# Optimization experiments

Hardware: AMD Instinct MI355X
Metric: run time of the kernel (lower is better)

## Reference

```python
import jax, jax.numpy as jnp
import numpy as np

BN_EPS = 1e-3
BN_SCALE = 1.0 / np.sqrt(1.0 + BN_EPS)  # inference BN with default moving stats (mean=0, var=1)


def _gru(x_seq, h0, Wx, Wh, b):
    """Keras GRU (reset_after=True). x_seq: [B,T,in], h0: [B,u].
    Wx: [in,3u], Wh: [u,3u], b: [2,3u] (input bias, recurrent bias).
    Returns (outputs [B,T,u], h_T [B,u])."""
    # precompute input contributions for all timesteps in one big matmul
    xg = jnp.einsum('bti,ig->btg', x_seq, Wx) + b[0]  # [B,T,3u]
    xg = jnp.moveaxis(xg, 1, 0)  # [T,B,3u] for scan

    def step(h, xt):
        rg = h @ Wh + b[1]  # [B,3u]
        xz, xr, xh = jnp.split(xt, 3, axis=-1)
        rz, rr, rh = jnp.split(rg, 3, axis=-1)
        z = jax.nn.sigmoid(xz + rz)
        r = jax.nn.sigmoid(xr + rr)
        hh = jnp.tanh(xh + r * rh)
        hn = z * h + (1.0 - z) * hh
        return hn, hn

    hT, ys = jax.lax.scan(step, h0, xg)
    return jnp.moveaxis(ys, 0, 1), hT  # [B,T,u], [B,u]


def _encoder(x_ids, h0, E, params):
    xcur = E[x_ids]  # [B,T,d]
    new_hidden = []
    out = xcur
    for i, (Wxf, Whf, bf, Wxb, Whb, bb) in enumerate(params):
        fw_out, fw_h = _gru(xcur, h0[i, 0], Wxf, Whf, bf)
        bw_out, bw_h = _gru(xcur[:, ::-1, :], h0[i, 1], Wxb, Whb, bb)
        # BN(training=False) with fresh layers == scale by 1/sqrt(1+eps)
        out = jnp.concatenate([fw_out * BN_SCALE, bw_out * BN_SCALE], axis=2)
        new_hidden.append(jnp.stack([fw_h, bw_h], axis=0))
        xcur = out
    # final BN on each direction hidden state
    new_hidden = jnp.stack(new_hidden, axis=0) * BN_SCALE  # [L,2,B,u]
    return out, new_hidden


def setup_inputs() -> dict:
    key = jax.random.key(0)
    ks = jax.random.split(key, 16)
    B, T, V, D, U = 32, 256, 32000, 512, 512
    s = 0.1
    inp = {
        'x': jax.random.randint(ks[0], (B, T), 0, V, dtype=jnp.int64)
             if jax.config.jax_enable_x64 else jax.random.randint(ks[0], (B, T), 0, V, dtype=jnp.int32),
        'h0': jnp.zeros((2, 2, B, U), jnp.float32),
        'E': jax.random.normal(ks[1], (V, D), jnp.float32) * s,
        'Wx0f': jax.random.normal(ks[2], (D, 3 * U), jnp.float32) * s,
        'Wh0f': jax.random.normal(ks[3], (U, 3 * U), jnp.float32) * s,
        'b0f': jax.random.normal(ks[4], (2, 3 * U), jnp.float32) * s,
        'Wx0b': jax.random.normal(ks[5], (D, 3 * U), jnp.float32) * s,
        'Wh0b': jax.random.normal(ks[6], (U, 3 * U), jnp.float32) * s,
        'b0b': jax.random.normal(ks[7], (2, 3 * U), jnp.float32) * s,
        'Wx1f': jax.random.normal(ks[8], (2 * U, 3 * U), jnp.float32) * s,
        'Wh1f': jax.random.normal(ks[9], (U, 3 * U), jnp.float32) * s,
        'b1f': jax.random.normal(ks[10], (2, 3 * U), jnp.float32) * s,
        'Wx1b': jax.random.normal(ks[11], (2 * U, 3 * U), jnp.float32) * s,
        'Wh1b': jax.random.normal(ks[12], (U, 3 * U), jnp.float32) * s,
        'b1b': jax.random.normal(ks[13], (2, 3 * U), jnp.float32) * s,
    }
    return inp


def reference(x, h0, E, Wx0f, Wh0f, b0f, Wx0b, Wh0b, b0b,
              Wx1f, Wh1f, b1f, Wx1b, Wh1b, b1b):
    params = [(Wx0f, Wh0f, b0f, Wx0b, Wh0b, b0b),
              (Wx1f, Wh1f, b1f, Wx1b, Wh1b, b1b)]
    return _encoder(x, h0, E, params)
```

## Files before the change

kernel.cpp:

```cpp
#include <hip/hip_runtime.h>
#include <hip/hip_bf16.h>


typedef __attribute__((ext_vector_type(8))) short short8;
typedef __attribute__((ext_vector_type(8))) __bf16 bf16x8;
typedef __attribute__((ext_vector_type(4))) float f32x4;
typedef __attribute__((ext_vector_type(4))) int i32x4;
typedef __attribute__((ext_vector_type(2))) float f32x2;

#define DEVINLINE __device__ __forceinline__

static constexpr int B = 32, T = 256, U = 512, NG = 1536;
static constexpr int BU = B * U;
static constexpr long OUT_ELEMS = 8388608;
static constexpr float SCALE_BN = 0.9995003746879552f;

DEVINLINE unsigned bfbits(float f) {
  unsigned u = __float_as_uint(f);
  return (u + 0x7fffu + ((u >> 16) & 1u)) >> 16;
}
DEVINLINE float bf2f(unsigned bits) { return __uint_as_float(bits << 16); }
DEVINLINE void split2(float v, unsigned& hi, unsigned& lo) {
  hi = bfbits(v);
  lo = bfbits(v - bf2f(hi));
}
DEVINLINE float sigmoidf_(float x) { return 1.f / (1.f + __expf(-x)); }
DEVINLINE float tanhf_(float x) {
  x = fminf(15.f, fmaxf(-15.f, x));
  float e = __expf(2.f * x);
  return (e - 1.f) / (e + 1.f);
}
DEVINLINE f32x4 mfma16(short8 a, short8 b, f32x4 c) {
  return __builtin_amdgcn_mfma_f32_16x16x32_bf16(
      __builtin_bit_cast(bf16x8, a), __builtin_bit_cast(bf16x8, b), c, 0, 0, 0);
}

__global__ __launch_bounds__(256)
void transpose_w(const float* __restrict__ in, unsigned short* __restrict__ oh,
                 unsigned short* __restrict__ ol, int K, int N) {
  __shared__ float tile[32][33];
  const int n0 = blockIdx.x * 32, k0 = blockIdx.y * 32;
  const int tx = threadIdx.x & 31, ty = threadIdx.x >> 5;
  for (int i = ty; i < 32; i += 8)
    tile[i][tx] = in[(long)(k0 + i) * N + n0 + tx];
  __syncthreads();
  for (int i = ty; i < 32; i += 8) {
    const float v = tile[tx][i];
    unsigned hi, lo;
    split2(v, hi, lo);
    oh[(long)(n0 + i) * K + k0 + tx] = (unsigned short)hi;
    ol[(long)(n0 + i) * K + k0 + tx] = (unsigned short)lo;
  }
}

__global__ __launch_bounds__(256)
void embed_kernel(const int* __restrict__ x, const float* __restrict__ E,
                  unsigned short* __restrict__ xh, unsigned short* __restrict__ xl) {
  const int r = blockIdx.x;
  const int t = r >> 5, b = r & 31;
  const int id = x[b * T + t];
  const float* src = E + (long)id * 512;
  f32x2 v = *reinterpret_cast<const f32x2*>(src + threadIdx.x * 2);
  unsigned h0, l0, h1, l1;
  split2(v.x, h0, l0);
  split2(v.y, h1, l1);
  ((unsigned*)xh)[(long)r * 256 + threadIdx.x] = h0 | (h1 << 16);
  ((unsigned*)xl)[(long)r * 256 + threadIdx.x] = l0 | (l1 << 16);
}

template <int K>
__global__ __launch_bounds__(256)
void gemm_bias(const unsigned short* __restrict__ Ah,
               const unsigned short* __restrict__ Al,
               const unsigned short* __restrict__ Bh,
               const unsigned short* __restrict__ Bl,
               const float* __restrict__ bias, float* __restrict__ C) {
  __shared__ __align__(16) unsigned short AsH[128 * 32];
  __shared__ __align__(16) unsigned short BsH[128 * 32];
  __shared__ __align__(16) unsigned short AsL[128 * 32];
  __shared__ __align__(16) unsigned short BsL[128 * 32];
  const int m0 = blockIdx.x * 128, n0 = blockIdx.y * 128;
  const int tid = threadIdx.x, lane = tid & 63, wave = tid >> 6;
  const int wr = wave >> 1, wc = wave & 1, lr = lane & 15, kq = lane >> 4;
  f32x4 acc[4][4] = {};
  for (int kt = 0; kt < K / 32; ++kt) {
    const int k0 = kt * 32;
    i32x4 vah[2], vbh[2], val[2], vbl[2];
#pragma unroll
    for (int u = 0; u < 2; ++u) {
      const int idx = tid + u * 256, row = idx >> 2, sub = idx & 3;
      vah[u] = *reinterpret_cast<const i32x4*>(Ah + (long)(m0 + row) * K + k0 + sub * 8);
      vbh[u] = *reinterpret_cast<const i32x4*>(Bh + (long)(n0 + row) * K + k0 + sub * 8);
      val[u] = *reinterpret_cast<const i32x4*>(Al + (long)(m0 + row) * K + k0 + sub * 8);
      vbl[u] = *reinterpret_cast<const i32x4*>(Bl + (long)(n0 + row) * K + k0 + sub * 8);
    }
    __syncthreads();
#pragma unroll
    for (int u = 0; u < 2; ++u) {
      const int idx = tid + u * 256;
      *reinterpret_cast<i32x4*>(AsH + idx * 8) = vah[u];
      *reinterpret_cast<i32x4*>(BsH + idx * 8) = vbh[u];
      *reinterpret_cast<i32x4*>(AsL + idx * 8) = val[u];
      *reinterpret_cast<i32x4*>(BsL + idx * 8) = vbl[u];
    }
    __syncthreads();
    short8 afh[4], bfh[4], afl[4], bfl[4];
#pragma unroll
    for (int i = 0; i < 4; ++i) {
      afh[i] = *reinterpret_cast<const short8*>(AsH + (wr * 64 + i * 16 + lr) * 32 + kq * 8);
      bfh[i] = *reinterpret_cast<const short8*>(BsH + (wc * 64 + i * 16 + lr) * 32 + kq * 8);
      afl[i] = *reinterpret_cast<const short8*>(AsL + (wr * 64 + i * 16 + lr) * 32 + kq * 8);
      bfl[i] = *reinterpret_cast<const short8*>(BsL + (wc * 64 + i * 16 + lr) * 32 + kq * 8);
    }
#pragma unroll
    for (int i = 0; i < 4; ++i)
#pragma unroll
      for (int j = 0; j < 4; ++j) {
        acc[i][j] = mfma16(afh[i], bfh[j], acc[i][j]);
        acc[i][j] = mfma16(afh[i], bfl[j], acc[i][j]);
        acc[i][j] = mfma16(afl[i], bfh[j], acc[i][j]);
      }
  }
#pragma unroll
  for (int j = 0; j < 4; ++j) {
    const int col = n0 + wc * 64 + j * 16 + lr;
    const float bv = bias[col];
#pragma unroll
    for (int i = 0; i < 4; ++i) {
      const int row0 = m0 + wr * 64 + i * 16 + kq * 4;
#pragma unroll
      for (int r = 0; r < 4; ++r)
        C[(long)(row0 + r) * NG + col] = acc[i][j][r] + bv;
    }
  }
}

__global__ __launch_bounds__(384, 1)
void gru_scan(const float* __restrict__ xgf, const float* __restrict__ xgb,
              const unsigned short* __restrict__ whtfh,
              const unsigned short* __restrict__ whtfl,
              const unsigned short* __restrict__ whtbh,
              const unsigned short* __restrict__ whtbl,
              const float* __restrict__ rbf, const float* __restrict__ rbb,
              const float* __restrict__ h0L,
              unsigned short* __restrict__ hbh,
              unsigned short* __restrict__ hbl,
              int* __restrict__ flags,
              unsigned short* __restrict__ out0h,
              unsigned short* __restrict__ out0l,
              float* __restrict__ outF,
              float* __restrict__ hT,
              const int layer) {
  const int dir = blockIdx.x >> 4, wg = blockIdx.x & 15;
  const int j0 = wg * 32;
  const int tid = threadIdx.x, wave = tid >> 6, lane = tid & 63;
  const int lr = lane & 15, kq = lane >> 4;
  const float* xg = dir ? xgb : xgf;
  const unsigned short* wth = dir ? whtbh : whtfh;
  const unsigned short* wtl = dir ? whtbl : whtfl;
  const float* rb = dir ? rbb : rbf;
  const float* h0d = h0L + dir * BU;
  unsigned short* hbhd = hbh + dir * 2 * BU;
  unsigned short* hbld = hbl + dir * 2 * BU;
  int* flg = flags + dir * 16;

  __shared__ __align__(16) unsigned short h_hi[32][520];
  __shared__ __align__(16) unsigned short h_lo[32][520];
  __shared__ float rg_lds[32][97];

  const int g = wave >> 1, half = wave & 1;
  const int c0 = g * 512 + j0 + half * 16;
  short8 wfh[16], wfl[16];
#pragma unroll
  for (int kk = 0; kk < 16; ++kk) {
    wfh[kk] = *reinterpret_cast<const short8*>(wth + (long)(c0 + lr) * 512 + kk * 32 + kq * 8);
    wfl[kk] = *reinterpret_cast<const short8*>(wtl + (long)(c0 + lr) * 512 + kk * 32 + kq * 8);
  }
  const float bv = rb[c0 + lr];

  float hpr[2][2];
#pragma unroll
  for (int q = 0; q < 2; ++q) {
    const int p = tid + q * 384;
    if (p < 512) {
      const int b = p >> 4, jr = (p & 15) * 2;
      hpr[q][0] = h0d[b * U + j0 + jr];
      hpr[q][1] = h0d[b * U + j0 + jr + 1];
    }
  }

  for (int s = 0; s < T; ++s) {
    const int t_in = dir ? (T - 1 - s) : s;
    const int par = s & 1;

    f32x2 xv[2][3];
    {
      const long xbase = (long)t_in * 32 * NG;
#pragma unroll
      for (int q = 0; q < 2; ++q) {
        const int p = tid + q * 384;
        if (p < 512) {
          const int b = p >> 4, jr = (p & 15) * 2;
#pragma unroll
          for (int gg = 0; gg < 3; ++gg)
            xv[q][gg] = *reinterpret_cast<const f32x2*>(
                xg + xbase + (long)b * NG + gg * 512 + j0 + jr);
        }
      }
    }

    if (s == 0) {
      for (int p = tid; p < BU / 4; p += 384) {
        const int b = p >> 7, u = (p & 127) * 4;
        f32x4 v = *reinterpret_cast<const f32x4*>(h0d + b * U + u);
        unsigned hi0, lo0, hi1, lo1, hi2, lo2, hi3, lo3;
        split2(v.x, hi0, lo0); split2(v.y, hi1, lo1);
        split2(v.z, hi2, lo2); split2(v.w, hi3, lo3);
        unsigned* dh = reinterpret_cast<unsigned*>(&h_hi[b][u]);
        unsigned* dl = reinterpret_cast<unsigned*>(&h_lo[b][u]);
        dh[0] = hi0 | (hi1 << 16); dh[1] = hi2 | (hi3 << 16);
        dl[0] = lo0 | (lo1 << 16); dl[1] = lo2 | (lo3 << 16);
      }
    } else {
      const unsigned short* hsh = hbhd + par * BU;
      const unsigned short* hsl = hbld + par * BU;
      for (int p = tid; p < BU / 8; p += 384) {
        const int b = p >> 6, u = (p & 63) * 8;
        *reinterpret_cast<i32x4*>(&h_hi[b][u]) =
            *reinterpret_cast<const i32x4*>(hsh + b * U + u);
        *reinterpret_cast<i32x4*>(&h_lo[b][u]) =
            *reinterpret_cast<const i32x4*>(hsl + b * U + u);
      }
    }
    __syncthreads();

    f32x4 aHH0 = {}, aHL0 = {}, aLH0 = {}, aHH1 = {}, aHL1 = {}, aLH1 = {};
#pragma unroll
    for (int kk = 0; kk < 16; ++kk) {
      const short8 a0h = *reinterpret_cast<const short8*>(&h_hi[lr][kk * 32 + kq * 8]);
      const short8 a0l = *reinterpret_cast<const short8*>(&h_lo[lr][kk * 32 + kq * 8]);
      const short8 a1h = *reinterpret_cast<const short8*>(&h_hi[16 + lr][kk * 32 + kq * 8]);
      const short8 a1l = *reinterpret_cast<const short8*>(&h_lo[16 + lr][kk * 32 + kq * 8]);
      aHH0 = mfma16(a0h, wfh[kk], aHH0);
      aHL0 = mfma16(a0h, wfl[kk], aHL0);
      aLH0 = mfma16(a0l, wfh[kk], aLH0);
      aHH1 = mfma16(a1h, wfh[kk], aHH1);
      aHL1 = mfma16(a1h, wfl[kk], aHL1);
      aLH1 = mfma16(a1l, wfh[kk], aLH1);
    }
#pragma unroll
    for (int r = 0; r < 4; ++r) {
      rg_lds[kq * 4 + r][wave * 16 + lr] = aHH0[r] + aHL0[r] + aLH0[r] + bv;
      rg_lds[16 + kq * 4 + r][wave * 16 + lr] = aHH1[r] + aHL1[r] + aLH1[r] + bv;
    }
    __syncthreads();

    unsigned short* hdh = hbhd + (1 - par) * BU;
    unsigned short* hdl = hbld + (1 - par) * BU;
#pragma unroll
    for (int q = 0; q < 2; ++q) {
      const int p = tid + q * 384;
      if (p >= 512) break;
      const int b = p >> 4, jr = (p & 15) * 2;
      float hn[2];
#pragma unroll
      for (int e = 0; e < 2; ++e) {
        const int j = jr + e;
        const float xz = xv[q][0][e], xr = xv[q][1][e], xh = xv[q][2][e];
        const float rz = rg_lds[b][j], rr = rg_lds[b][32 + j], rh = rg_lds[b][64 + j];
        const float z = sigmoidf_(xz + rz);
        const float r = sigmoidf_(xr + rr);
        const float hh = tanhf_(xh + r * rh);
        hn[e] = z * hpr[q][e] + (1.f - z) * hh;
      }
      hpr[q][0] = hn[0];
      hpr[q][1] = hn[1];
      unsigned hi0, lo0, hi1, lo1;
      split2(hn[0], hi0, lo0); split2(hn[1], hi1, lo1);
      *reinterpret_cast<unsigned*>(hdh + b * U + j0 + jr) = hi0 | (hi1 << 16);
      *reinterpret_cast<unsigned*>(hdl + b * U + j0 + jr) = lo0 | (lo1 << 16);
      if (layer == 0) {
        const float o0 = hn[0] * SCALE_BN, o1 = hn[1] * SCALE_BN;
        unsigned oh0, ol0, oh1, ol1;
        split2(o0, oh0, ol0); split2(o1, oh1, ol1);
        const long oidx = (((long)s * 32 + b) * 1024 + dir * 512 + j0 + jr) >> 1;
        ((unsigned*)out0h)[oidx] = oh0 | (oh1 << 16);
        ((unsigned*)out0l)[oidx] = ol0 | (ol1 << 16);
      } else {
        float* o = outF + ((long)b * T + s) * 1024 + dir * 512 + j0 + jr;
        o[0] = hn[0] * SCALE_BN;
        o[1] = hn[1] * SCALE_BN;
      }
      if (s == T - 1) {
        float* o = hT + dir * BU + b * U + j0 + jr;
        o[0] = hn[0] * SCALE_BN;
        o[1] = hn[1] * SCALE_BN;
      }
    }
    __syncthreads();
    if (tid == 0)
      __hip_atomic_store(flg + wg, s + 1, __ATOMIC_RELEASE, __HIP_MEMORY_SCOPE_AGENT);
    if (s < T - 1) {
      if (tid < 16) {
        while (__hip_atomic_load(flg + tid, __ATOMIC_ACQUIRE, __HIP_MEMORY_SCOPE_AGENT) < s + 1)
          __builtin_amdgcn_s_sleep(2);
      }
      __syncthreads();
    }
  }
}

extern "C" void kernel_launch(void* const* d_in, const int* in_sizes, int n_in,
                              void* d_out, int out_size, void* d_ws, size_t ws_size,
                              hipStream_t stream) {
  (void)in_sizes; (void)n_in; (void)out_size; (void)ws_size;
  const int*   x    = (const int*)d_in[0];
  const float* h0   = (const float*)d_in[1];
  const float* E    = (const float*)d_in[2];
  const float* Wx0f = (const float*)d_in[3];
  const float* Wh0f = (const float*)d_in[4];
  const float* b0f  = (const float*)d_in[5];
  const float* Wx0b = (const float*)d_in[6];
  const float* Wh0b = (const float*)d_in[7];
  const float* b0b  = (const float*)d_in[8];
  const float* Wx1f = (const float*)d_in[9];
  const float* Wh1f = (const float*)d_in[10];
  const float* b1f  = (const float*)d_in[11];
  const float* Wx1b = (const float*)d_in[12];
  const float* Wh1b = (const float*)d_in[13];
  const float* b1b  = (const float*)d_in[14];
  float* dout = (float*)d_out;

  char* p = (char*)d_ws;
  auto alloc = [&p](long bytes) { char* r = p; p += (bytes + 255) & ~255L; return r; };
  float* XGF = (float*)alloc(50331648);
  float* XGB = (float*)alloc(50331648);
  unsigned short* OUT0H = (unsigned short*)alloc(16777216);
  unsigned short* OUT0L = (unsigned short*)alloc(16777216);
  unsigned short* X0H = OUT0H;
  unsigned short* X0L = OUT0L;
  unsigned short* WHT0FH = (unsigned short*)alloc(1572864);
  unsigned short* WHT0FL = (unsigned short*)alloc(1572864);
  unsigned short* WHT0BH = (unsigned short*)alloc(1572864);
  unsigned short* WHT0BL = (unsigned short*)alloc(1572864);
  unsigned short* WHT1FH = (unsigned short*)alloc(1572864);
  unsigned short* WHT1FL = (unsigned short*)alloc(1572864);
  unsigned short* WHT1BH = (unsigned short*)alloc(1572864);
  unsigned short* WHT1BL = (unsigned short*)alloc(1572864);
  unsigned short* WXT0FH = (unsigned short*)alloc(1572864);
  unsigned short* WXT0FL = (unsigned short*)alloc(1572864);
  unsigned short* WXT0BH = (unsigned short*)alloc(1572864);
  unsigned short* WXT0BL = (unsigned short*)alloc(1572864);
  unsigned short* WXT1FH = (unsigned short*)alloc(3145728);
  unsigned short* WXT1FL = (unsigned short*)alloc(3145728);
  unsigned short* WXT1BH = (unsigned short*)alloc(3145728);
  unsigned short* WXT1BL = (unsigned short*)alloc(3145728);
  unsigned short* HBH = (unsigned short*)alloc(131072);
  unsigned short* HBL = (unsigned short*)alloc(131072);
  int* FLAGS = (int*)alloc(256);

  hipMemsetAsync(FLAGS, 0, 256, stream);

  dim3 blk(256);
  transpose_w<<<dim3(48, 16), blk, 0, stream>>>(Wh0f, WHT0FH, WHT0FL, 512, NG);
  transpose_w<<<dim3(48, 16), blk, 0, stream>>>(Wh0b, WHT0BH, WHT0BL, 512, NG);
  transpose_w<<<dim3(48, 16), blk, 0, stream>>>(Wh1f, WHT1FH, WHT1FL, 512, NG);
  transpose_w<<<dim3(48, 16), blk, 0, stream>>>(Wh1b, WHT1BH, WHT1BL, 512, NG);
  transpose_w<<<dim3(48, 16), blk, 0, stream>>>(Wx0f, WXT0FH, WXT0FL, 512, NG);
  transpose_w<<<dim3(48, 16), blk, 0, stream>>>(Wx0b, WXT0BH, WXT0BL, 512, NG);
  transpose_w<<<dim3(48, 32), blk, 0, stream>>>(Wx1f, WXT1FH, WXT1FL, 1024, NG);
  transpose_w<<<dim3(48, 32), blk, 0, stream>>>(Wx1b, WXT1BH, WXT1BL, 1024, NG);

  embed_kernel<<<dim3(8192), blk, 0, stream>>>(x, E, X0H, X0L);

  gemm_bias<512><<<dim3(64, 12), blk, 0, stream>>>(
      X0H, X0L, WXT0FH, WXT0FL, b0f, XGF);
  gemm_bias<512><<<dim3(64, 12), blk, 0, stream>>>(
      X0H, X0L, WXT0BH, WXT0BL, b0b, XGB);
  gru_scan<<<dim3(32), dim3(384), 0, stream>>>(
      XGF, XGB, WHT0FH, WHT0FL, WHT0BH, WHT0BL, b0f + NG, b0b + NG, h0,
      HBH, HBL, FLAGS, OUT0H, OUT0L, nullptr, dout + OUT_ELEMS, 0);

  gemm_bias<1024><<<dim3(64, 12), blk, 0, stream>>>(
      OUT0H, OUT0L, WXT1FH, WXT1FL, b1f, XGF);
  gemm_bias<1024><<<dim3(64, 12), blk, 0, stream>>>(
      OUT0H, OUT0L, WXT1BH, WXT1BL, b1b, XGB);
  gru_scan<<<dim3(32), dim3(384), 0, stream>>>(
      XGF, XGB, WHT1FH, WHT1FL, WHT1BH, WHT1BL, b1f + NG, b1b + NG, h0 + 2 * BU,
      HBH, HBL, FLAGS + 32, nullptr, nullptr, dout, dout + OUT_ELEMS + 2 * BU, 1);
}
```

Measured before the change: 3.888 ms.

## Relax inter-block sync to relaxed atomics and prefetch next-step gate inputs

Replaces the release/acquire flag handshake with relaxed flag operations plus an explicit vmcnt wait. The shared hidden-state buffers are now written and read with relaxed agent-scope atomics, which is meant to avoid the cache writeback and invalidate costs of release/acquire on each of the 256 steps. It also prefetches the next timestep's input-gate values while waiting on the flags, shortens the spin sleep, and pads the LDS rows differently to change bank mapping. The risk is memory-ordering correctness: visibility of the hidden state across blocks now relies on atomic cache bypass behaviour rather than formal acquire/release semantics.

```diff
diff --git a/kernel.cpp b/kernel.cpp
--- a/kernel.cpp
+++ b/kernel.cpp
@@ -164,8 +164,8 @@
   unsigned short* hbld = hbl + dir * 2 * BU;
   int* flg = flags + dir * 16;
 
-  __shared__ __align__(16) unsigned short h_hi[32][520];
-  __shared__ __align__(16) unsigned short h_lo[32][520];
+  __shared__ __align__(16) unsigned short h_hi[32][544];
+  __shared__ __align__(16) unsigned short h_lo[32][544];
   __shared__ float rg_lds[32][97];
 
   const int g = wave >> 1, half = wave & 1;
@@ -189,25 +189,25 @@
     }
   }
 
+  f32x2 xv[2][3];
+  auto load_xv = [&](int t_in) {
+    const long xbase = (long)t_in * 32 * NG;
+#pragma unroll
+    for (int q = 0; q < 2; ++q) {
+      const int p = tid + q * 384;
+      if (p < 512) {
+        const int b = p >> 4, jr = (p & 15) * 2;
+#pragma unroll
+        for (int gg = 0; gg < 3; ++gg)
+          xv[q][gg] = *reinterpret_cast<const f32x2*>(
+              xg + xbase + (long)b * NG + gg * 512 + j0 + jr);
+      }
+    }
+  };
+  load_xv(dir ? (T - 1) : 0);
+
   for (int s = 0; s < T; ++s) {
-    const int t_in = dir ? (T - 1 - s) : s;
     const int par = s & 1;
-
-    f32x2 xv[2][3];
-    {
-      const long xbase = (long)t_in * 32 * NG;
-#pragma unroll
-      for (int q = 0; q < 2; ++q) {
-        const int p = tid + q * 384;
-        if (p < 512) {
-          const int b = p >> 4, jr = (p & 15) * 2;
-#pragma unroll
-          for (int gg = 0; gg < 3; ++gg)
-            xv[q][gg] = *reinterpret_cast<const f32x2*>(
-                xg + xbase + (long)b * NG + gg * 512 + j0 + jr);
-        }
-      }
-    }
 
     if (s == 0) {
       for (int p = tid; p < BU / 4; p += 384) {
@@ -222,14 +222,18 @@
         dl[0] = lo0 | (lo1 << 16); dl[1] = lo2 | (lo3 << 16);
       }
     } else {
-      const unsigned short* hsh = hbhd + par * BU;
-      const unsigned short* hsl = hbld + par * BU;
-      for (int p = tid; p < BU / 8; p += 384) {
-        const int b = p >> 6, u = (p & 63) * 8;
-        *reinterpret_cast<i32x4*>(&h_hi[b][u]) =
-            *reinterpret_cast<const i32x4*>(hsh + b * U + u);
-        *reinterpret_cast<i32x4*>(&h_lo[b][u]) =
-            *reinterpret_cast<const i32x4*>(hsl + b * U + u);
+      const unsigned long long* hsh =
+          (const unsigned long long*)(hbhd + par * BU);
+      const unsigned long long* hsl =
+          (const unsigned long long*)(hbld + par * BU);
+      for (int p = tid; p < BU / 4; p += 384) {
+        const int b = p >> 7, u = (p & 127) * 4;
+        unsigned long long vh = __hip_atomic_load(
+            hsh + (b * U + u) / 4, __ATOMIC_RELAXED, __HIP_MEMORY_SCOPE_AGENT);
+        unsigned long long vl = __hip_atomic_load(
+            hsl + (b * U + u) / 4, __ATOMIC_RELAXED, __HIP_MEMORY_SCOPE_AGENT);
+        *reinterpret_cast<unsigned long long*>(&h_hi[b][u]) = vh;
+        *reinterpret_cast<unsigned long long*>(&h_lo[b][u]) = vl;
       }
     }
     __syncthreads();
@@ -255,8 +259,8 @@
     }
     __syncthreads();
 
-    unsigned short* hdh = hbhd + (1 - par) * BU;
-    unsigned short* hdl = hbld + (1 - par) * BU;
+    unsigned* hdh = (unsigned*)(hbhd + (1 - par) * BU);
+    unsigned* hdl = (unsigned*)(hbld + (1 - par) * BU);
 #pragma unroll
     for (int q = 0; q < 2; ++q) {
       const int p = tid + q * 384;
@@ -277,8 +281,10 @@
       hpr[q][1] = hn[1];
       unsigned hi0, lo0, hi1, lo1;
       split2(hn[0], hi0, lo0); split2(hn[1], hi1, lo1);
-      *reinterpret_cast<unsigned*>(hdh + b * U + j0 + jr) = hi0 | (hi1 << 16);
-      *reinterpret_cast<unsigned*>(hdl + b * U + j0 + jr) = lo0 | (lo1 << 16);
+      __hip_atomic_store(hdh + (b * U + j0 + jr) / 2, hi0 | (hi1 << 16),
+                         __ATOMIC_RELAXED, __HIP_MEMORY_SCOPE_AGENT);
+      __hip_atomic_store(hdl + (b * U + j0 + jr) / 2, lo0 | (lo1 << 16),
+                         __ATOMIC_RELAXED, __HIP_MEMORY_SCOPE_AGENT);
       if (layer == 0) {
         const float o0 = hn[0] * SCALE_BN, o1 = hn[1] * SCALE_BN;
         unsigned oh0, ol0, oh1, ol1;
@@ -297,13 +303,15 @@
         o[1] = hn[1] * SCALE_BN;
       }
     }
+    asm volatile("s_waitcnt vmcnt(0)" ::: "memory");
     __syncthreads();
     if (tid == 0)
-      __hip_atomic_store(flg + wg, s + 1, __ATOMIC_RELEASE, __HIP_MEMORY_SCOPE_AGENT);
+      __hip_atomic_store(flg + wg, s + 1, __ATOMIC_RELAXED, __HIP_MEMORY_SCOPE_AGENT);
     if (s < T - 1) {
+      load_xv(dir ? (T - 2 - s) : (s + 1));
       if (tid < 16) {
-        while (__hip_atomic_load(flg + tid, __ATOMIC_ACQUIRE, __HIP_MEMORY_SCOPE_AGENT) < s + 1)
-          __builtin_amdgcn_s_sleep(2);
+        while (__hip_atomic_load(flg + tid, __ATOMIC_RELAXED, __HIP_MEMORY_SCOPE_AGENT) < s + 1)
+          __builtin_amdgcn_s_sleep(1);
       }
       __syncthreads();
     }
```

Result: slower. 3.972 ms (+2.2%).
